# Performance work log

Hardware: AMD Instinct MI355X
Metric: run time of the kernel (lower is better)

## Reference

```python
import jax, jax.numpy as jnp
import numpy as np

B, S, L, F = 4, 4, 1024, 256
D, H = 256, 8
DH = D // H


def setup_inputs() -> dict:
    key = jax.random.key(0)
    ks = jax.random.split(key, 9)
    scale = 0.06  # ~1/sqrt(fan_in) init scale
    return {
        "x": jax.random.normal(ks[0], (B, S, L, F), dtype=jnp.float32),
        "Wq": jax.random.normal(ks[1], (D, F), dtype=jnp.float32) * scale,
        "bq": jnp.zeros((D,), dtype=jnp.float32),
        "Wk": jax.random.normal(ks[2], (D, F), dtype=jnp.float32) * scale,
        "bk": jnp.zeros((D,), dtype=jnp.float32),
        "Wv": jax.random.normal(ks[3], (D, F), dtype=jnp.float32) * scale,
        "bv": jnp.zeros((D,), dtype=jnp.float32),
        "Wo": jax.random.normal(ks[4], (D, D), dtype=jnp.float32) * scale,
        "bo": jnp.zeros((D,), dtype=jnp.float32),
    }


def reference(x, Wq, bq, Wk, bk, Wv, bv, Wo, bo):
    b, s, l, f = x.shape
    xr = x.reshape(b * s, l, f)  # [N, L, F] with N = batch*samples

    def split_heads(t):  # [N, L, D] -> [N, H, L, DH]
        return t.reshape(b * s, l, H, DH).transpose(0, 2, 1, 3)

    q = split_heads(xr @ Wq.T + bq)
    k = split_heads(xr @ Wk.T + bk)
    v = split_heads(xr @ Wv.T + bv)

    scores = jnp.einsum("nhqd,nhkd->nhqk", q, k) / jnp.sqrt(jnp.float32(DH))
    probs = jax.nn.softmax(scores, axis=-1)  # [N, H, L, L] — materialized as in original
    out = jnp.einsum("nhqk,nhkd->nhqd", probs, v)

    out = out.transpose(0, 2, 1, 3).reshape(b * s, l, D)
    out = out @ Wo.T + bo
    out = out.reshape(b, s, l, D)

    # softmax pooling over seq_len (dim=2)
    weight = jax.nn.softmax(out, axis=2)
    return jnp.sum(out * weight, axis=2)  # [B, S, D]
```

## Files before the change

### kernel.cpp

```cpp
#include <hip/hip_runtime.h>
#include <math.h>

#define N_SEQ 16
#define LEN   1024
#define FDIM  256
#define DDIM  256
#define NHEAD 8
#define DHD   32
#define ROWS  (N_SEQ * LEN)
#define QSCALE 0.17677669529663687f
#define QKVN  ((size_t)N_SEQ * NHEAD * LEN * DHD)

typedef __attribute__((ext_vector_type(8))) short bf16x8;
typedef __attribute__((ext_vector_type(4))) float f32x4;

__device__ __forceinline__ unsigned short f2bf(float f) {
    unsigned int u = __float_as_uint(f);
    unsigned int r = u + 0x7fffu + ((u >> 16) & 1u);
    return (unsigned short)(r >> 16);
}

__global__ __launch_bounds__(256) void convert_bf16(
    const float* __restrict__ X,
    const float* __restrict__ Wq, const float* __restrict__ Wk,
    const float* __restrict__ Wv, const float* __restrict__ Wo,
    unsigned short* __restrict__ Xbf, unsigned short* __restrict__ Wbf)
{
    const size_t idx4 = ((size_t)blockIdx.x * 256 + threadIdx.x) * 4;
    const float* src;
    unsigned short* dst;
    if (idx4 < (size_t)ROWS * FDIM) {
        src = X + idx4;
        dst = Xbf + idx4;
    } else {
        const size_t wi = idx4 - (size_t)ROWS * FDIM;
        const int w = (int)(wi >> 16);
        const size_t off = wi & 65535;
        const float* Ws[4] = {Wq, Wk, Wv, Wo};
        src = Ws[w] + off;
        dst = Wbf + wi;
    }
    float4 v = *(const float4*)src;
    ushort4 u;
    u.x = f2bf(v.x); u.y = f2bf(v.y); u.z = f2bf(v.z); u.w = f2bf(v.w);
    *(ushort4*)dst = u;
}

#define LDT 72
template <int MODE>
__global__ __launch_bounds__(256) void gemm_bf16(
    const unsigned short* __restrict__ Ag, const unsigned short* __restrict__ Bg,
    const float* __restrict__ b0, const float* __restrict__ b1,
    const float* __restrict__ b2,
    unsigned short* __restrict__ OutB,
    float* __restrict__ pmO, float* __restrict__ plO, float* __restrict__ psO)
{
    __shared__ unsigned short As[128 * LDT];
    __shared__ unsigned short Bs[128 * LDT];

    const int m0 = blockIdx.x * 128;
    const int n0 = blockIdx.y * 128;
    const int tid  = threadIdx.x;
    const int wv   = tid >> 6;
    const int lane = tid & 63;
    const int l15  = lane & 15;
    const int quad = lane >> 4;
    const int wr = (wv & 1) * 64;
    const int wc = (wv >> 1) * 64;
    const int srow = tid >> 3;
    const int sc8  = (tid & 7) * 8;

    f32x4 acc[4][4] = {};

    for (int kt = 0; kt < 4; ++kt) {
        __syncthreads();
        #pragma unroll
        for (int i = 0; i < 4; ++i) {
            const int row = i * 32 + srow;
            *(bf16x8*)(&As[row * LDT + sc8]) =
                *(const bf16x8*)(Ag + (size_t)(m0 + row) * 256 + kt * 64 + sc8);
            *(bf16x8*)(&Bs[row * LDT + sc8]) =
                *(const bf16x8*)(Bg + (size_t)(n0 + row) * 256 + kt * 64 + sc8);
        }
        __syncthreads();
        #pragma unroll
        for (int ks = 0; ks < 2; ++ks) {
            bf16x8 af[4], bfr[4];
            #pragma unroll
            for (int i = 0; i < 4; ++i)
                af[i] = *(const bf16x8*)(&As[(wr + i*16 + l15) * LDT + ks*32 + quad*8]);
            #pragma unroll
            for (int j = 0; j < 4; ++j)
                bfr[j] = *(const bf16x8*)(&Bs[(wc + j*16 + l15) * LDT + ks*32 + quad*8]);
            #pragma unroll
            for (int i = 0; i < 4; ++i)
                #pragma unroll
                for (int j = 0; j < 4; ++j)
                    acc[i][j] = __builtin_amdgcn_mfma_f32_16x16x32_bf16(
                        af[i], bfr[j], acc[i][j], 0, 0, 0);
        }
    }

    if (MODE == 0) {
        const int mat = n0 >> 8;
        const float scale = (mat == 0) ? QSCALE : 1.0f;
        const float* __restrict__ bias = (mat == 0) ? b0 : (mat == 1) ? b1 : b2;
        unsigned short* __restrict__ Out = OutB + (size_t)mat * QKVN;
        #pragma unroll
        for (int j = 0; j < 4; ++j) {
            const int c  = n0 + wc + j*16 + l15;
            const int cc = c & 255;
            const int h = cc >> 5, dh = cc & 31;
            const float bv = bias[cc];
            #pragma unroll
            for (int i = 0; i < 4; ++i)
                #pragma unroll
                for (int rr = 0; rr < 4; ++rr) {
                    const int r = m0 + wr + i*16 + quad*4 + rr;
                    const int n = r >> 10, l = r & 1023;
                    Out[(((size_t)(n*NHEAD + h)) * LEN + l) * DHD + dh] =
                        f2bf((acc[i][j][rr] + bv) * scale);
                }
        }
    } else {
        const int n    = blockIdx.x >> 3;
        const int tile = blockIdx.x & 7;
        __shared__ float red[4][64];

        float bv[4];
        #pragma unroll
        for (int j = 0; j < 4; ++j) bv[j] = b0[n0 + wc + j*16 + l15];
        #pragma unroll
        for (int i = 0; i < 4; ++i)
            #pragma unroll
            for (int j = 0; j < 4; ++j)
                #pragma unroll
                for (int rr = 0; rr < 4; ++rr)
                    acc[i][j][rr] += bv[j];

        float M[4];
        #pragma unroll
        for (int j = 0; j < 4; ++j) {
            float m = -1e30f;
            #pragma unroll
            for (int i = 0; i < 4; ++i)
                #pragma unroll
                for (int rr = 0; rr < 4; ++rr) m = fmaxf(m, acc[i][j][rr]);
            m = fmaxf(m, __shfl_xor(m, 16));
            m = fmaxf(m, __shfl_xor(m, 32));
            M[j] = m;
        }
        if (quad == 0) {
            #pragma unroll
            for (int j = 0; j < 4; ++j) red[wv][j*16 + l15] = M[j];
        }
        __syncthreads();
        #pragma unroll
        for (int j = 0; j < 4; ++j)
            M[j] = fmaxf(red[wv][j*16 + l15], red[wv^1][j*16 + l15]);
        __syncthreads();

        float LE[4], SE[4];
        #pragma unroll
        for (int j = 0; j < 4; ++j) {
            float le = 0.f, se = 0.f;
            #pragma unroll
            for (int i = 0; i < 4; ++i)
                #pragma unroll
                for (int rr = 0; rr < 4; ++rr) {
                    const float z = acc[i][j][rr];
                    const float e = __expf(z - M[j]);
                    le += e; se += z * e;
                }
            le += __shfl_xor(le, 16); le += __shfl_xor(le, 32);
            se += __shfl_xor(se, 16); se += __shfl_xor(se, 32);
            LE[j] = le; SE[j] = se;
        }
        if (quad == 0) {
            #pragma unroll
            for (int j = 0; j < 4; ++j) red[wv][j*16 + l15] = LE[j];
        }
        __syncthreads();
        float LEp[4];
        #pragma unroll
        for (int j = 0; j < 4; ++j) LEp[j] = red[wv^1][j*16 + l15];
        __syncthreads();
        if (quad == 0) {
            #pragma unroll
            for (int j = 0; j < 4; ++j) red[wv][j*16 + l15] = SE[j];
        }
        __syncthreads();
        float SEp[4];
        #pragma unroll
        for (int j = 0; j < 4; ++j) SEp[j] = red[wv^1][j*16 + l15];

        if ((wv & 1) == 0 && quad == 0) {
            #pragma unroll
            for (int j = 0; j < 4; ++j) {
                const int c = n0 + wc + j*16 + l15;
                const size_t o = ((size_t)n*8 + tile)*256 + c;
                pmO[o] = M[j];
                plO[o] = LE[j] + LEp[j];
                psO[o] = SE[j] + SEp[j];
            }
        }
    }
}

__global__ __launch_bounds__(256) void vtrans(
    const unsigned short* __restrict__ Vb, unsigned short* __restrict__ Vtb)
{
    __shared__ unsigned short Ls[64 * 34];

    const int nh = blockIdx.y;
    const int l0 = blockIdx.x * 64;
    const int tid = threadIdx.x;

    const int row = tid >> 2, c8 = (tid & 3) * 8;
    *(bf16x8*)(&Ls[row*34 + c8]) =
        *(const bf16x8*)(Vb + ((size_t)nh * LEN + l0 + row) * DHD + c8);
    __syncthreads();

    const int dh = tid >> 3, l8 = (tid & 7) * 8;
    ushort4 u0, u1;
    u0.x = Ls[(l8+0)*34 + dh]; u0.y = Ls[(l8+1)*34 + dh];
    u0.z = Ls[(l8+2)*34 + dh]; u0.w = Ls[(l8+3)*34 + dh];
    u1.x = Ls[(l8+4)*34 + dh]; u1.y = Ls[(l8+5)*34 + dh];
    u1.z = Ls[(l8+6)*34 + dh]; u1.w = Ls[(l8+7)*34 + dh];
    unsigned short* dst = Vtb + ((size_t)nh * DHD + dh) * LEN + l0 + l8;
    *(ushort4*)(dst)     = u0;
    *(ushort4*)(dst + 4) = u1;
}

#define LDK2 40
#define LDV2 136
#define LDPb 72
__global__ __launch_bounds__(256) void attn_mfma(
    const unsigned short* __restrict__ Qg_, const unsigned short* __restrict__ Kg_,
    const unsigned short* __restrict__ Vg_, unsigned short* __restrict__ Aout)
{
    __shared__ unsigned short Ks[128 * LDK2];
    __shared__ unsigned short Vs[32 * LDV2];
    __shared__ unsigned short Pb[4][16 * LDPb];
    __shared__ float stats[4][16];

    const int nh = blockIdx.y;
    const int n  = nh >> 3, h = nh & 7;
    const int q0 = blockIdx.x * 64;
    const int tid  = threadIdx.x;
    const int wv   = tid >> 6;
    const int lane = tid & 63;
    const int l15  = lane & 15;
    const int quad = lane >> 4;

    const unsigned short* __restrict__ Qg = Qg_ + (size_t)nh * LEN * DHD;
    const unsigned short* __restrict__ Kg = Kg_ + (size_t)nh * LEN * DHD;
    const unsigned short* __restrict__ Vg = Vg_ + (size_t)nh * DHD * LEN;

    bf16x8 qf = *(const bf16x8*)(Qg + (size_t)(q0 + wv*16 + l15) * DHD + quad*8);

    f32x4 o0 = {0.f, 0.f, 0.f, 0.f};
    f32x4 o1 = {0.f, 0.f, 0.f, 0.f};
    float l_lane[4] = {0.f, 0.f, 0.f, 0.f};

    const int krow = tid >> 2, kc8 = (tid & 3) * 8;
    const int vrow = tid >> 3, vc8 = (tid & 7) * 8;

    unsigned short* __restrict__ Pw = &Pb[wv][0];

    for (int kt = 0; kt < LEN / 128; ++kt) {
        const int k0 = kt * 128;
        __syncthreads();
        *(bf16x8*)(&Ks[krow*LDK2 + kc8]) =
            *(const bf16x8*)(Kg + (size_t)(k0 + krow)*DHD + kc8);
        *(bf16x8*)(&Ks[(64 + krow)*LDK2 + kc8]) =
            *(const bf16x8*)(Kg + (size_t)(k0 + 64 + krow)*DHD + kc8);
        *(bf16x8*)(&Vs[vrow*LDV2 + vc8]) =
            *(const bf16x8*)(Vg + (size_t)vrow*LEN + k0 + vc8);
        *(bf16x8*)(&Vs[vrow*LDV2 + 64 + vc8]) =
            *(const bf16x8*)(Vg + (size_t)vrow*LEN + k0 + 64 + vc8);
        __syncthreads();

        #pragma unroll
        for (int half = 0; half < 2; ++half) {
            f32x4 s[4];
            #pragma unroll
            for (int sub = 0; sub < 4; ++sub) {
                bf16x8 kf = *(const bf16x8*)(&Ks[(half*64 + sub*16 + l15)*LDK2 + quad*8]);
                f32x4 z = {0.f, 0.f, 0.f, 0.f};
                s[sub] = __builtin_amdgcn_mfma_f32_16x16x32_bf16(qf, kf, z, 0, 0, 0);
            }
            #pragma unroll
            for (int sub = 0; sub < 4; ++sub)
                #pragma unroll
                for (int r = 0; r < 4; ++r) {
                    const float p = __expf(s[sub][r]);
                    l_lane[r] += p;
                    Pw[(quad*4 + r)*LDPb + sub*16 + l15] = f2bf(p);
                }
            #pragma unroll
            for (int kk = 0; kk < 2; ++kk) {
                bf16x8 pf = *(const bf16x8*)(&Pw[l15*LDPb + kk*32 + quad*8]);
                bf16x8 va = *(const bf16x8*)(&Vs[l15*LDV2 + half*64 + kk*32 + quad*8]);
                bf16x8 vb = *(const bf16x8*)(&Vs[(16 + l15)*LDV2 + half*64 + kk*32 + quad*8]);
                o0 = __builtin_amdgcn_mfma_f32_16x16x32_bf16(va, pf, o0, 0, 0, 0);
                o1 = __builtin_amdgcn_mfma_f32_16x16x32_bf16(vb, pf, o1, 0, 0, 0);
            }
        }
    }

    #pragma unroll
    for (int r = 0; r < 4; ++r) {
        float t = l_lane[r];
        t += __shfl_xor(t, 1);
        t += __shfl_xor(t, 2);
        t += __shfl_xor(t, 4);
        t += __shfl_xor(t, 8);
        l_lane[r] = t;
    }
    __syncthreads();
    if (l15 == 0) {
        #pragma unroll
        for (int r = 0; r < 4; ++r) stats[wv][quad*4 + r] = l_lane[r];
    }
    __syncthreads();
    const float linv = 1.f / stats[wv][l15];

    float* __restrict__ Tw = (float*)&Pb[wv][0];
    #pragma unroll
    for (int r = 0; r < 4; ++r) {
        Tw[l15*36 + quad*4 + r]      = o0[r] * linv;
        Tw[l15*36 + 16 + quad*4 + r] = o1[r] * linv;
    }
    __syncthreads();
    const int qr = lane >> 2, c8 = (lane & 3) * 8;
    float4 r0 = *(const float4*)(&Tw[qr*36 + c8]);
    float4 r1 = *(const float4*)(&Tw[qr*36 + c8 + 4]);
    unsigned short* dst = Aout + ((size_t)(n*LEN + q0 + wv*16 + qr)) * DDIM + h*DHD + c8;
    ushort4 u0, u1;
    u0.x = f2bf(r0.x); u0.y = f2bf(r0.y); u0.z = f2bf(r0.z); u0.w = f2bf(r0.w);
    u1.x = f2bf(r1.x); u1.y = f2bf(r1.y); u1.z = f2bf(r1.z); u1.w = f2bf(r1.w);
    *(ushort4*)(dst)     = u0;
    *(ushort4*)(dst + 4) = u1;
}

__global__ __launch_bounds__(256) void pool_merge(
    const float* __restrict__ pm, const float* __restrict__ pl,
    const float* __restrict__ ps, float* __restrict__ out)
{
    const int n = blockIdx.x;
    const int d = threadIdx.x;
    float M = -1e30f;
    #pragma unroll
    for (int t = 0; t < 8; ++t) M = fmaxf(M, pm[((size_t)n*8 + t)*256 + d]);
    float L = 0.f, S = 0.f;
    #pragma unroll
    for (int t = 0; t < 8; ++t) {
        const size_t idx = ((size_t)n*8 + t)*256 + d;
        const float w = __expf(pm[idx] - M);
        L += pl[idx] * w;
        S += ps[idx] * w;
    }
    out[n*256 + d] = S / L;
}

extern "C" void kernel_launch(void* const* d_in, const int* in_sizes, int n_in,
                              void* d_out, int out_size, void* d_ws, size_t ws_size,
                              hipStream_t stream)
{
    const float* x  = (const float*)d_in[0];
    const float* Wq = (const float*)d_in[1];
    const float* bq = (const float*)d_in[2];
    const float* Wk = (const float*)d_in[3];
    const float* bk = (const float*)d_in[4];
    const float* Wv = (const float*)d_in[5];
    const float* bv = (const float*)d_in[6];
    const float* Wo = (const float*)d_in[7];
    const float* bo = (const float*)d_in[8];
    float* out = (float*)d_out;

    char* base = (char*)d_ws;
    unsigned short* Xbf  = (unsigned short*)(base);
    unsigned short* Qb   = (unsigned short*)(base +  8388608);
    unsigned short* Kb   = (unsigned short*)(base + 16777216);
    unsigned short* Vb   = (unsigned short*)(base + 25165824);
    unsigned short* Vtb  = (unsigned short*)(base + 33554432);
    unsigned short* attnb= (unsigned short*)(base + 41943040);
    unsigned short* Wbf  = (unsigned short*)(base + 50331648);
    float* pm = (float*)(base + 50855936);
    float* pl = (float*)(base + 50987008);
    float* ps = (float*)(base + 51118080);
    const size_t need_bytes = 51249152;
    if (ws_size < need_bytes) return;

    convert_bf16<<<4352, 256, 0, stream>>>(x, Wq, Wk, Wv, Wo, Xbf, Wbf);
    gemm_bf16<0><<<dim3(ROWS/128, 6), 256, 0, stream>>>(
        Xbf, Wbf, bq, bk, bv, Qb, nullptr, nullptr, nullptr);
    vtrans<<<dim3(LEN/64, N_SEQ*NHEAD), 256, 0, stream>>>(Vb, Vtb);
    attn_mfma<<<dim3(LEN/64, N_SEQ*NHEAD), 256, 0, stream>>>(Qb, Kb, Vtb, attnb);
    gemm_bf16<1><<<dim3(ROWS/128, 2), 256, 0, stream>>>(
        attnb, Wbf + (size_t)768*256, bo, nullptr, nullptr, nullptr, pm, pl, ps);
    pool_merge<<<16, 256, 0, stream>>>(pm, pl, ps, out);
}
```

Measured before the change: 158.4 us.

## Use direct global-to-LDS loads in GEMM and register-direct K/V in attention

The GEMM tiles are now loaded with global_load_lds straight into a fragment-ordered LDS layout, so the VGPR round trip and padded-row staging go away and the MFMA operand reads become contiguous per lane. The attention kernel drops its shared K/V tiles and block barriers. Each wave reads its K and V fragments directly from global memory (L2-cached), and K is prefetched one 64-key block ahead. The aim is lower synchronization and LDS traffic. The cost is redundant global reads of K/V across the four waves and more exposed memory latency.

```diff
diff --git a/kernel.cpp b/kernel.cpp
--- a/kernel.cpp
+++ b/kernel.cpp
@@ -18,6 +18,12 @@
     unsigned int u = __float_as_uint(f);
     unsigned int r = u + 0x7fffu + ((u >> 16) & 1u);
     return (unsigned short)(r >> 16);
+}
+
+__device__ __forceinline__ void load_lds16(const void* g, void* l) {
+    __builtin_amdgcn_global_load_lds(
+        (const __attribute__((address_space(1))) unsigned int*)g,
+        (__attribute__((address_space(3))) unsigned int*)l, 16, 0, 0);
 }
 
 __global__ __launch_bounds__(256) void convert_bf16(
@@ -46,7 +52,6 @@
     *(ushort4*)dst = u;
 }
 
-#define LDT 72
 template <int MODE>
 __global__ __launch_bounds__(256) void gemm_bf16(
     const unsigned short* __restrict__ Ag, const unsigned short* __restrict__ Bg,
@@ -55,8 +60,8 @@
     unsigned short* __restrict__ OutB,
     float* __restrict__ pmO, float* __restrict__ plO, float* __restrict__ psO)
 {
-    __shared__ unsigned short As[128 * LDT];
-    __shared__ unsigned short Bs[128 * LDT];
+    __shared__ unsigned short As[16 * 512];
+    __shared__ unsigned short Bs[16 * 512];
 
     const int m0 = blockIdx.x * 128;
     const int n0 = blockIdx.y * 128;
@@ -67,20 +72,23 @@
     const int quad = lane >> 4;
     const int wr = (wv & 1) * 64;
     const int wc = (wv >> 1) * 64;
-    const int srow = tid >> 3;
-    const int sc8  = (tid & 7) * 8;
+
+    const int isB = wv >> 1;
+    const unsigned short* __restrict__ Mg = isB ? Bg : Ag;
+    const int mb0 = isB ? n0 : m0;
+    unsigned short* Ms = isB ? Bs : As;
+    const int fbase = (wv & 1) * 8;
 
     f32x4 acc[4][4] = {};
 
     for (int kt = 0; kt < 4; ++kt) {
         __syncthreads();
         #pragma unroll
-        for (int i = 0; i < 4; ++i) {
-            const int row = i * 32 + srow;
-            *(bf16x8*)(&As[row * LDT + sc8]) =
-                *(const bf16x8*)(Ag + (size_t)(m0 + row) * 256 + kt * 64 + sc8);
-            *(bf16x8*)(&Bs[row * LDT + sc8]) =
-                *(const bf16x8*)(Bg + (size_t)(n0 + row) * 256 + kt * 64 + sc8);
+        for (int f = 0; f < 8; ++f) {
+            const int fi = fbase + f;
+            const int i = fi >> 1, ks = fi & 1;
+            load_lds16(Mg + (size_t)(mb0 + i*16 + l15) * 256 + kt*64 + ks*32 + quad*8,
+                       Ms + fi * 512);
         }
         __syncthreads();
         #pragma unroll
@@ -88,10 +96,10 @@
             bf16x8 af[4], bfr[4];
             #pragma unroll
             for (int i = 0; i < 4; ++i)
-                af[i] = *(const bf16x8*)(&As[(wr + i*16 + l15) * LDT + ks*32 + quad*8]);
+                af[i] = *(const bf16x8*)(&As[((((wv & 1)*4 + i)*2) + ks)*512 + lane*8]);
             #pragma unroll
             for (int j = 0; j < 4; ++j)
-                bfr[j] = *(const bf16x8*)(&Bs[(wc + j*16 + l15) * LDT + ks*32 + quad*8]);
+                bfr[j] = *(const bf16x8*)(&Bs[((((wv >> 1)*4 + j)*2) + ks)*512 + lane*8]);
             #pragma unroll
             for (int i = 0; i < 4; ++i)
                 #pragma unroll
@@ -232,15 +240,11 @@
     *(ushort4*)(dst + 4) = u1;
 }
 
-#define LDK2 40
-#define LDV2 136
 #define LDPb 72
 __global__ __launch_bounds__(256) void attn_mfma(
     const unsigned short* __restrict__ Qg_, const unsigned short* __restrict__ Kg_,
     const unsigned short* __restrict__ Vg_, unsigned short* __restrict__ Aout)
 {
-    __shared__ unsigned short Ks[128 * LDK2];
-    __shared__ unsigned short Vs[32 * LDV2];
     __shared__ unsigned short Pb[4][16 * LDPb];
     __shared__ float stats[4][16];
 
@@ -259,53 +263,49 @@
 
     bf16x8 qf = *(const bf16x8*)(Qg + (size_t)(q0 + wv*16 + l15) * DHD + quad*8);
 
+    const unsigned short* __restrict__ krow = Kg + (size_t)l15 * DHD + quad*8;
+    const unsigned short* __restrict__ varow = Vg + (size_t)l15 * LEN;
+    const unsigned short* __restrict__ vbrow = Vg + (size_t)(16 + l15) * LEN;
+
     f32x4 o0 = {0.f, 0.f, 0.f, 0.f};
     f32x4 o1 = {0.f, 0.f, 0.f, 0.f};
     float l_lane[4] = {0.f, 0.f, 0.f, 0.f};
 
-    const int krow = tid >> 2, kc8 = (tid & 3) * 8;
-    const int vrow = tid >> 3, vc8 = (tid & 7) * 8;
-
     unsigned short* __restrict__ Pw = &Pb[wv][0];
 
-    for (int kt = 0; kt < LEN / 128; ++kt) {
-        const int k0 = kt * 128;
-        __syncthreads();
-        *(bf16x8*)(&Ks[krow*LDK2 + kc8]) =
-            *(const bf16x8*)(Kg + (size_t)(k0 + krow)*DHD + kc8);
-        *(bf16x8*)(&Ks[(64 + krow)*LDK2 + kc8]) =
-            *(const bf16x8*)(Kg + (size_t)(k0 + 64 + krow)*DHD + kc8);
-        *(bf16x8*)(&Vs[vrow*LDV2 + vc8]) =
-            *(const bf16x8*)(Vg + (size_t)vrow*LEN + k0 + vc8);
-        *(bf16x8*)(&Vs[vrow*LDV2 + 64 + vc8]) =
-            *(const bf16x8*)(Vg + (size_t)vrow*LEN + k0 + 64 + vc8);
-        __syncthreads();
-
-        #pragma unroll
-        for (int half = 0; half < 2; ++half) {
-            f32x4 s[4];
-            #pragma unroll
-            for (int sub = 0; sub < 4; ++sub) {
-                bf16x8 kf = *(const bf16x8*)(&Ks[(half*64 + sub*16 + l15)*LDK2 + quad*8]);
-                f32x4 z = {0.f, 0.f, 0.f, 0.f};
-                s[sub] = __builtin_amdgcn_mfma_f32_16x16x32_bf16(qf, kf, z, 0, 0, 0);
+    bf16x8 kf[4];
+    #pragma unroll
+    for (int sub = 0; sub < 4; ++sub)
+        kf[sub] = *(const bf16x8*)(krow + (size_t)(sub*16) * DHD);
+
+    for (int kb = 0; kb < 16; ++kb) {
+        const int k0 = kb * 64;
+        f32x4 s[4];
+        #pragma unroll
+        for (int sub = 0; sub < 4; ++sub) {
+            f32x4 z = {0.f, 0.f, 0.f, 0.f};
+            s[sub] = __builtin_amdgcn_mfma_f32_16x16x32_bf16(qf, kf[sub], z, 0, 0, 0);
+        }
+        if (kb < 15) {
+            #pragma unroll
+            for (int sub = 0; sub < 4; ++sub)
+                kf[sub] = *(const bf16x8*)(krow + (size_t)(k0 + 64 + sub*16) * DHD);
+        }
+        #pragma unroll
+        for (int sub = 0; sub < 4; ++sub)
+            #pragma unroll
+            for (int r = 0; r < 4; ++r) {
+                const float p = __expf(s[sub][r]);
+                l_lane[r] += p;
+                Pw[(quad*4 + r)*LDPb + sub*16 + l15] = f2bf(p);
             }
-            #pragma unroll
-            for (int sub = 0; sub < 4; ++sub)
-                #pragma unroll
-                for (int r = 0; r < 4; ++r) {
-                    const float p = __expf(s[sub][r]);
-                    l_lane[r] += p;
-                    Pw[(quad*4 + r)*LDPb + sub*16 + l15] = f2bf(p);
-                }
-            #pragma unroll
-            for (int kk = 0; kk < 2; ++kk) {
-                bf16x8 pf = *(const bf16x8*)(&Pw[l15*LDPb + kk*32 + quad*8]);
-                bf16x8 va = *(const bf16x8*)(&Vs[l15*LDV2 + half*64 + kk*32 + quad*8]);
-                bf16x8 vb = *(const bf16x8*)(&Vs[(16 + l15)*LDV2 + half*64 + kk*32 + quad*8]);
-                o0 = __builtin_amdgcn_mfma_f32_16x16x32_bf16(va, pf, o0, 0, 0, 0);
-                o1 = __builtin_amdgcn_mfma_f32_16x16x32_bf16(vb, pf, o1, 0, 0, 0);
-            }
+        #pragma unroll
+        for (int kk = 0; kk < 2; ++kk) {
+            bf16x8 pf = *(const bf16x8*)(&Pw[l15*LDPb + kk*32 + quad*8]);
+            bf16x8 va = *(const bf16x8*)(varow + k0 + kk*32 + quad*8);
+            bf16x8 vb = *(const bf16x8*)(vbrow + k0 + kk*32 + quad*8);
+            o0 = __builtin_amdgcn_mfma_f32_16x16x32_bf16(va, pf, o0, 0, 0, 0);
+            o1 = __builtin_amdgcn_mfma_f32_16x16x32_bf16(vb, pf, o1, 0, 0, 0);
         }
     }
 
```

After: 199.5 us. 1.26x slower.

## Use direct global-to-LDS loads in GEMM and transpose score MFMA in attention

Applied to the files above, without the earlier changes.

The GEMM staging now uses global_load_lds 16-byte transfers straight into LDS, which avoids the register round trip. The tiles are laid out in fragment order so each lane reads its MFMA operand at a contiguous lane*8 offset, and half the waves load A while the other half load B. In attention the QK MFMA operands are swapped, so each lane holds four consecutive keys for one query. P can then be written as packed 8-byte stores, and the row sum reduces with two cross-quad shuffles instead of a shuffle tree, an LDS stats buffer and two barriers. The risks are that the fragment layout may cause LDS bank conflicts and that global_load_lds depends on the compiler and the hardware.

```diff
diff --git a/kernel.cpp b/kernel.cpp
--- a/kernel.cpp
+++ b/kernel.cpp
@@ -18,6 +18,12 @@
     unsigned int u = __float_as_uint(f);
     unsigned int r = u + 0x7fffu + ((u >> 16) & 1u);
     return (unsigned short)(r >> 16);
+}
+
+__device__ __forceinline__ void load_lds16(const void* g, void* l) {
+    __builtin_amdgcn_global_load_lds(
+        (const __attribute__((address_space(1))) unsigned int*)g,
+        (__attribute__((address_space(3))) unsigned int*)l, 16, 0, 0);
 }
 
 __global__ __launch_bounds__(256) void convert_bf16(
@@ -46,7 +52,6 @@
     *(ushort4*)dst = u;
 }
 
-#define LDT 72
 template <int MODE>
 __global__ __launch_bounds__(256) void gemm_bf16(
     const unsigned short* __restrict__ Ag, const unsigned short* __restrict__ Bg,
@@ -55,8 +60,8 @@
     unsigned short* __restrict__ OutB,
     float* __restrict__ pmO, float* __restrict__ plO, float* __restrict__ psO)
 {
-    __shared__ unsigned short As[128 * LDT];
-    __shared__ unsigned short Bs[128 * LDT];
+    __shared__ unsigned short As[16 * 512];
+    __shared__ unsigned short Bs[16 * 512];
 
     const int m0 = blockIdx.x * 128;
     const int n0 = blockIdx.y * 128;
@@ -67,20 +72,23 @@
     const int quad = lane >> 4;
     const int wr = (wv & 1) * 64;
     const int wc = (wv >> 1) * 64;
-    const int srow = tid >> 3;
-    const int sc8  = (tid & 7) * 8;
+
+    const int isB = wv >> 1;
+    const unsigned short* __restrict__ Mg = isB ? Bg : Ag;
+    const int mb0 = isB ? n0 : m0;
+    unsigned short* Ms = isB ? Bs : As;
+    const int fbase = (wv & 1) * 8;
 
     f32x4 acc[4][4] = {};
 
     for (int kt = 0; kt < 4; ++kt) {
         __syncthreads();
         #pragma unroll
-        for (int i = 0; i < 4; ++i) {
-            const int row = i * 32 + srow;
-            *(bf16x8*)(&As[row * LDT + sc8]) =
-                *(const bf16x8*)(Ag + (size_t)(m0 + row) * 256 + kt * 64 + sc8);
-            *(bf16x8*)(&Bs[row * LDT + sc8]) =
-                *(const bf16x8*)(Bg + (size_t)(n0 + row) * 256 + kt * 64 + sc8);
+        for (int f = 0; f < 8; ++f) {
+            const int fi = fbase + f;
+            const int i = fi >> 1, ks = fi & 1;
+            load_lds16(Mg + (size_t)(mb0 + i*16 + l15) * 256 + kt*64 + ks*32 + quad*8,
+                       Ms + fi * 512);
         }
         __syncthreads();
         #pragma unroll
@@ -88,10 +96,10 @@
             bf16x8 af[4], bfr[4];
             #pragma unroll
             for (int i = 0; i < 4; ++i)
-                af[i] = *(const bf16x8*)(&As[(wr + i*16 + l15) * LDT + ks*32 + quad*8]);
+                af[i] = *(const bf16x8*)(&As[((((wv & 1)*4 + i)*2) + ks)*512 + lane*8]);
             #pragma unroll
             for (int j = 0; j < 4; ++j)
-                bfr[j] = *(const bf16x8*)(&Bs[(wc + j*16 + l15) * LDT + ks*32 + quad*8]);
+                bfr[j] = *(const bf16x8*)(&Bs[((((wv >> 1)*4 + j)*2) + ks)*512 + lane*8]);
             #pragma unroll
             for (int i = 0; i < 4; ++i)
                 #pragma unroll
@@ -234,15 +242,14 @@
 
 #define LDK2 40
 #define LDV2 136
-#define LDPb 72
+#define LDPk 72
 __global__ __launch_bounds__(256) void attn_mfma(
     const unsigned short* __restrict__ Qg_, const unsigned short* __restrict__ Kg_,
     const unsigned short* __restrict__ Vg_, unsigned short* __restrict__ Aout)
 {
     __shared__ unsigned short Ks[128 * LDK2];
     __shared__ unsigned short Vs[32 * LDV2];
-    __shared__ unsigned short Pb[4][16 * LDPb];
-    __shared__ float stats[4][16];
+    __shared__ unsigned short Pb[4][16 * LDPk];
 
     const int nh = blockIdx.y;
     const int n  = nh >> 3, h = nh & 7;
@@ -261,7 +268,7 @@
 
     f32x4 o0 = {0.f, 0.f, 0.f, 0.f};
     f32x4 o1 = {0.f, 0.f, 0.f, 0.f};
-    float l_lane[4] = {0.f, 0.f, 0.f, 0.f};
+    float l_lane = 0.f;
 
     const int krow = tid >> 2, kc8 = (tid & 3) * 8;
     const int vrow = tid >> 3, vc8 = (tid & 7) * 8;
@@ -283,24 +290,28 @@
 
         #pragma unroll
         for (int half = 0; half < 2; ++half) {
-            f32x4 s[4];
+            f32x4 st[4];
             #pragma unroll
             for (int sub = 0; sub < 4; ++sub) {
                 bf16x8 kf = *(const bf16x8*)(&Ks[(half*64 + sub*16 + l15)*LDK2 + quad*8]);
                 f32x4 z = {0.f, 0.f, 0.f, 0.f};
-                s[sub] = __builtin_amdgcn_mfma_f32_16x16x32_bf16(qf, kf, z, 0, 0, 0);
+                st[sub] = __builtin_amdgcn_mfma_f32_16x16x32_bf16(kf, qf, z, 0, 0, 0);
             }
             #pragma unroll
-            for (int sub = 0; sub < 4; ++sub)
-                #pragma unroll
-                for (int r = 0; r < 4; ++r) {
-                    const float p = __expf(s[sub][r]);
-                    l_lane[r] += p;
-                    Pw[(quad*4 + r)*LDPb + sub*16 + l15] = f2bf(p);
-                }
+            for (int sub = 0; sub < 4; ++sub) {
+                const float p0 = __expf(st[sub][0]);
+                const float p1 = __expf(st[sub][1]);
+                const float p2 = __expf(st[sub][2]);
+                const float p3 = __expf(st[sub][3]);
+                l_lane += (p0 + p1) + (p2 + p3);
+                uint2 pk;
+                pk.x = (unsigned int)f2bf(p0) | ((unsigned int)f2bf(p1) << 16);
+                pk.y = (unsigned int)f2bf(p2) | ((unsigned int)f2bf(p3) << 16);
+                *(uint2*)(&Pw[l15*LDPk + sub*16 + quad*4]) = pk;
+            }
             #pragma unroll
             for (int kk = 0; kk < 2; ++kk) {
-                bf16x8 pf = *(const bf16x8*)(&Pw[l15*LDPb + kk*32 + quad*8]);
+                bf16x8 pf = *(const bf16x8*)(&Pw[l15*LDPk + kk*32 + quad*8]);
                 bf16x8 va = *(const bf16x8*)(&Vs[l15*LDV2 + half*64 + kk*32 + quad*8]);
                 bf16x8 vb = *(const bf16x8*)(&Vs[(16 + l15)*LDV2 + half*64 + kk*32 + quad*8]);
                 o0 = __builtin_amdgcn_mfma_f32_16x16x32_bf16(va, pf, o0, 0, 0, 0);
@@ -309,22 +320,9 @@
         }
     }
 
-    #pragma unroll
-    for (int r = 0; r < 4; ++r) {
-        float t = l_lane[r];
-        t += __shfl_xor(t, 1);
-        t += __shfl_xor(t, 2);
-        t += __shfl_xor(t, 4);
-        t += __shfl_xor(t, 8);
-        l_lane[r] = t;
-    }
-    __syncthreads();
-    if (l15 == 0) {
-        #pragma unroll
-        for (int r = 0; r < 4; ++r) stats[wv][quad*4 + r] = l_lane[r];
-    }
-    __syncthreads();
-    const float linv = 1.f / stats[wv][l15];
+    l_lane += __shfl_xor(l_lane, 16);
+    l_lane += __shfl_xor(l_lane, 32);
+    const float linv = 1.f / l_lane;
 
     float* __restrict__ Tw = (float*)&Pb[wv][0];
     #pragma unroll
```

Result: no change. 159.8 us (+0.9%).
